# Kernel tuning notes

Measured on AMD Instinct MI355X. Metric: run time of the kernel, lower is better.

## Reference

```python
import jax, jax.numpy as jnp
import numpy as np

HAAR_K = 6  # kernel_size

def _haar_kernels_2d(k):
    # 6 classic Haar-like 2D kernels, each normalized by k*k (matches fixed
    # HaarFeatures2d conv weights): full box, 2-rect edges (h/v), 3-rect
    # lines (h/v), 4-rect checker.
    n = float(k * k)
    ks = []
    w = np.ones((k, k), np.float32); ks.append(w.copy())                      # full box
    w = np.ones((k, k), np.float32); w[k // 2:, :] = -1.0; ks.append(w)       # 2-rect vertical split
    w = np.ones((k, k), np.float32); w[:, k // 2:] = -1.0; ks.append(w)       # 2-rect horizontal split
    t = k // 3
    w = np.ones((k, k), np.float32); w[t:k - t, :] = -1.0; ks.append(w)       # 3-rect line (rows)
    w = np.ones((k, k), np.float32); w[:, t:k - t] = -1.0; ks.append(w)       # 3-rect line (cols)
    w = np.ones((k, k), np.float32)
    w[:k // 2, k // 2:] = -1.0; w[k // 2:, :k // 2] = -1.0; ks.append(w)      # 4-rect checker
    return jnp.asarray(np.stack(ks) / n)  # [6, k, k]


def setup_inputs() -> dict:
    key = jax.random.key(0)
    ks = jax.random.split(key, 4)
    def lin(k, o, i):  # kaiming-ish 1x1 conv weight as [out, in]
        return jax.random.normal(k, (o, i), jnp.float32) * (1.0 / np.sqrt(i))
    return {
        "x": jax.random.normal(ks[0], (16, 1, 512, 512), jnp.float32),
        "w1": lin(ks[1], 32, 6),  "b1": jnp.zeros((32,), jnp.float32),
        "w2": lin(ks[2], 16, 32), "b2": jnp.zeros((16,), jnp.float32),
        "w3": lin(ks[3], 2, 16),  "b3": jnp.zeros((2,), jnp.float32),
    }


def reference(x, w1, b1, w2, b2, w3, b3):
    # Fixed Haar-like feature extraction: conv with 6 constant kernels,
    # stride 1, 'same' zero padding. x: [B,1,H,W] -> f: [B,6,H,W]
    hk = _haar_kernels_2d(HAAR_K)[:, None]  # [6,1,k,k] OIHW
    f = jax.lax.conv_general_dilated(
        x, hk, window_strides=(1, 1), padding='SAME',
        dimension_numbers=('NCHW', 'OIHW', 'NCHW'))
    # 1x1-conv MLP classifier (Dropout2d is identity at inference)
    h = jax.nn.relu(jnp.einsum('bchw,oc->bohw', f, w1) + b1[None, :, None, None])
    h = jax.nn.relu(jnp.einsum('bchw,oc->bohw', h, w2) + b2[None, :, None, None])
    return jnp.einsum('bchw,oc->bohw', h, w3) + b3[None, :, None, None]  # [B,2,H,W]
```

## Files before the change

### kernel.cpp

```cpp
#include <hip/hip_runtime.h>


#define TW 64
#define TH 16

__global__ __launch_bounds__(512) void haar_prep(const float* __restrict__ w1,
                                                 const float* __restrict__ b1,
                                                 const float* __restrict__ w2,
                                                 float* __restrict__ ws) {
  int t = threadIdx.x;
  if (t < 256) {
    int m = t >> 3, k = t & 7;
    float v = 0.f;
    if (k < 6) v = w1[m * 6 + k] * (1.0f / 36.0f);
    else if (k == 6) v = b1[m];
    ws[t] = v;
  }
  int m = t >> 4, o = t & 15;
  ws[256 + t] = w2[o * 32 + m];
}

__global__ __launch_bounds__(256) void haar_main(const float* __restrict__ x,
                                                 const float* __restrict__ ws,
                                                 const float* __restrict__ b2,
                                                 const float* __restrict__ w3,
                                                 const float* __restrict__ b3,
                                                 float* __restrict__ out) {
  __shared__ float tile[TH + 5][72];

  const int tid = threadIdx.x;
  const int bc = blockIdx.x * TW;
  const int br = blockIdx.y * TH;
  const int b  = blockIdx.z;
  const float* xb = x + (size_t)b * (512 * 512);

  #pragma unroll
  for (int e = 0; e < 6; ++e) {
    int idx = tid + e * 256;
    if (idx < (TH + 5) * (TW + 5)) {
      int r = idx / (TW + 5);
      int c = idx - r * (TW + 5);
      int gr = br - 2 + r, gc = bc - 2 + c;
      float v = 0.f;
      if ((unsigned)gr < 512u && (unsigned)gc < 512u) v = xb[gr * 512 + gc];
      tile[r][c] = v;
    }
  }
  __syncthreads();

  const int jl = tid & 63;
  const int r0 = (tid >> 6) * 4;

  float A[9], S[9], T[9];
  #pragma unroll
  for (int rr = 0; rr < 9; ++rr) {
    const float* row = &tile[r0 + rr][jl];
    float x0 = row[0], x1 = row[1], x2 = row[2];
    float x3 = row[3], x4 = row[4], x5 = row[5];
    float p01 = x0 + x1, p23 = x2 + x3, p45 = x4 + x5;
    A[rr] = p01 + p23 + p45;
    T[rr] = p01 - p23 + p45;
    S[rr] = (p01 + x2) - (x3 + p45);
  }

  float f[6][4];
  #pragma unroll
  for (int p = 0; p < 4; ++p) {
    float ta = A[p] + A[p + 1] + A[p + 2];
    float tb = A[p + 3] + A[p + 4] + A[p + 5];
    f[0][p] = ta + tb;
    f[1][p] = ta - tb;
    float q01 = A[p] + A[p + 1], q23 = A[p + 2] + A[p + 3], q45 = A[p + 4] + A[p + 5];
    f[3][p] = q01 - q23 + q45;
    float sa = S[p] + S[p + 1] + S[p + 2];
    float sb = S[p + 3] + S[p + 4] + S[p + 5];
    f[2][p] = sa + sb;
    f[5][p] = sa - sb;
    f[4][p] = ((T[p] + T[p + 1]) + (T[p + 2] + T[p + 3])) + (T[p + 4] + T[p + 5]);
  }

  float h2[16][4];
  #pragma unroll
  for (int o = 0; o < 16; ++o) {
    float bv = b2[o];
    #pragma unroll
    for (int p = 0; p < 4; ++p) h2[o][p] = bv;
  }

  for (int m = 0; m < 32; ++m) {
    const float* pw1 = ws + m * 8;
    float w0 = pw1[0], w1v = pw1[1], w2v = pw1[2];
    float w3v = pw1[3], w4v = pw1[4], w5v = pw1[5], b1v = pw1[6];
    float t[4];
    #pragma unroll
    for (int p = 0; p < 4; ++p) {
      float a = fmaf(w0, f[0][p], b1v);
      a = fmaf(w1v, f[1][p], a);
      a = fmaf(w2v, f[2][p], a);
      a = fmaf(w3v, f[3][p], a);
      a = fmaf(w4v, f[4][p], a);
      a = fmaf(w5v, f[5][p], a);
      t[p] = fmaxf(a, 0.f);
    }
    const float* pw2 = ws + 256 + m * 16;
    #pragma unroll
    for (int o = 0; o < 16; ++o) {
      float wv = pw2[o];
      #pragma unroll
      for (int p = 0; p < 4; ++p) h2[o][p] = fmaf(wv, t[p], h2[o][p]);
    }
  }

  #pragma unroll
  for (int p = 0; p < 4; ++p) {
    float r[16];
    #pragma unroll
    for (int o = 0; o < 16; ++o) r[o] = fmaxf(h2[o][p], 0.f);
    #pragma unroll
    for (int u = 0; u < 2; ++u) {
      float acc = b3[u];
      #pragma unroll
      for (int o = 0; o < 16; ++o) acc = fmaf(w3[u * 16 + o], r[o], acc);
      size_t oidx = (((size_t)(b * 2 + u) * 512) + (br + r0 + p)) * 512 + (bc + jl);
      out[oidx] = acc;
    }
  }
}

extern "C" void kernel_launch(void* const* d_in, const int* in_sizes, int n_in,
                              void* d_out, int out_size, void* d_ws, size_t ws_size,
                              hipStream_t stream) {
  const float* x  = (const float*)d_in[0];
  const float* w1 = (const float*)d_in[1];
  const float* b1 = (const float*)d_in[2];
  const float* w2 = (const float*)d_in[3];
  const float* b2 = (const float*)d_in[4];
  const float* w3 = (const float*)d_in[5];
  const float* b3 = (const float*)d_in[6];
  float* out = (float*)d_out;
  float* ws  = (float*)d_ws;

  haar_prep<<<1, 512, 0, stream>>>(w1, b1, w2, ws);

  dim3 grid(512 / TW, 512 / TH, 16);
  haar_main<<<grid, 256, 0, stream>>>(x, ws, b2, w3, b3, out);
}
```

Measured before the change: 85.77 us.

## Process MLP per pixel sequentially and interleave weights into one workspace record

After: 87.41 us. About the same (+1.9%).

```diff
diff --git a/kernel.cpp b/kernel.cpp
--- a/kernel.cpp
+++ b/kernel.cpp
@@ -4,20 +4,17 @@
 #define TW 64
 #define TH 16
 
-__global__ __launch_bounds__(512) void haar_prep(const float* __restrict__ w1,
+__global__ __launch_bounds__(768) void haar_prep(const float* __restrict__ w1,
                                                  const float* __restrict__ b1,
                                                  const float* __restrict__ w2,
                                                  float* __restrict__ ws) {
   int t = threadIdx.x;
-  if (t < 256) {
-    int m = t >> 3, k = t & 7;
-    float v = 0.f;
-    if (k < 6) v = w1[m * 6 + k] * (1.0f / 36.0f);
-    else if (k == 6) v = b1[m];
-    ws[t] = v;
-  }
-  int m = t >> 4, o = t & 15;
-  ws[256 + t] = w2[o * 32 + m];
+  int m = t / 24, j = t % 24;
+  float v = 0.f;
+  if (j < 6)       v = w1[m * 6 + j] * (1.0f / 36.0f);
+  else if (j == 6) v = b1[m];
+  else if (j >= 8) v = w2[(j - 8) * 32 + m];
+  ws[m * 24 + j] = v;
 }
 
 __global__ __launch_bounds__(256) void haar_main(const float* __restrict__ x,
@@ -63,67 +60,56 @@
     S[rr] = (p01 + x2) - (x3 + p45);
   }
 
-  float f[6][4];
+  float f[4][6];
   #pragma unroll
   for (int p = 0; p < 4; ++p) {
     float ta = A[p] + A[p + 1] + A[p + 2];
     float tb = A[p + 3] + A[p + 4] + A[p + 5];
-    f[0][p] = ta + tb;
-    f[1][p] = ta - tb;
+    f[p][0] = ta + tb;
+    f[p][1] = ta - tb;
     float q01 = A[p] + A[p + 1], q23 = A[p + 2] + A[p + 3], q45 = A[p + 4] + A[p + 5];
-    f[3][p] = q01 - q23 + q45;
+    f[p][3] = q01 - q23 + q45;
     float sa = S[p] + S[p + 1] + S[p + 2];
     float sb = S[p + 3] + S[p + 4] + S[p + 5];
-    f[2][p] = sa + sb;
-    f[5][p] = sa - sb;
-    f[4][p] = ((T[p] + T[p + 1]) + (T[p + 2] + T[p + 3])) + (T[p + 4] + T[p + 5]);
+    f[p][2] = sa + sb;
+    f[p][5] = sa - sb;
+    f[p][4] = ((T[p] + T[p + 1]) + (T[p + 2] + T[p + 3])) + (T[p + 4] + T[p + 5]);
   }
 
-  float h2[16][4];
-  #pragma unroll
-  for (int o = 0; o < 16; ++o) {
-    float bv = b2[o];
-    #pragma unroll
-    for (int p = 0; p < 4; ++p) h2[o][p] = bv;
-  }
-
-  for (int m = 0; m < 32; ++m) {
-    const float* pw1 = ws + m * 8;
-    float w0 = pw1[0], w1v = pw1[1], w2v = pw1[2];
-    float w3v = pw1[3], w4v = pw1[4], w5v = pw1[5], b1v = pw1[6];
-    float t[4];
-    #pragma unroll
-    for (int p = 0; p < 4; ++p) {
-      float a = fmaf(w0, f[0][p], b1v);
-      a = fmaf(w1v, f[1][p], a);
-      a = fmaf(w2v, f[2][p], a);
-      a = fmaf(w3v, f[3][p], a);
-      a = fmaf(w4v, f[4][p], a);
-      a = fmaf(w5v, f[5][p], a);
-      t[p] = fmaxf(a, 0.f);
-    }
-    const float* pw2 = ws + 256 + m * 16;
-    #pragma unroll
-    for (int o = 0; o < 16; ++o) {
-      float wv = pw2[o];
-      #pragma unroll
-      for (int p = 0; p < 4; ++p) h2[o][p] = fmaf(wv, t[p], h2[o][p]);
-    }
-  }
+  const int colg = bc + jl;
 
   #pragma unroll
   for (int p = 0; p < 4; ++p) {
-    float r[16];
+    float h2[16];
     #pragma unroll
-    for (int o = 0; o < 16; ++o) r[o] = fmaxf(h2[o][p], 0.f);
+    for (int o = 0; o < 16; ++o) h2[o] = b2[o];
+
+    #pragma unroll 2
+    for (int m = 0; m < 32; ++m) {
+      const float* pm = ws + m * 24;
+      float a = pm[6];
+      a = fmaf(pm[0], f[p][0], a);
+      a = fmaf(pm[1], f[p][1], a);
+      a = fmaf(pm[2], f[p][2], a);
+      a = fmaf(pm[3], f[p][3], a);
+      a = fmaf(pm[4], f[p][4], a);
+      a = fmaf(pm[5], f[p][5], a);
+      a = fmaxf(a, 0.f);
+      #pragma unroll
+      for (int o = 0; o < 16; ++o) h2[o] = fmaf(pm[8 + o], a, h2[o]);
+    }
+
+    float acc0 = b3[0], acc1 = b3[1];
     #pragma unroll
-    for (int u = 0; u < 2; ++u) {
-      float acc = b3[u];
-      #pragma unroll
-      for (int o = 0; o < 16; ++o) acc = fmaf(w3[u * 16 + o], r[o], acc);
-      size_t oidx = (((size_t)(b * 2 + u) * 512) + (br + r0 + p)) * 512 + (bc + jl);
-      out[oidx] = acc;
+    for (int o = 0; o < 16; ++o) {
+      float r = fmaxf(h2[o], 0.f);
+      acc0 = fmaf(w3[o], r, acc0);
+      acc1 = fmaf(w3[16 + o], r, acc1);
     }
+
+    const int row = br + r0 + p;
+    out[((size_t)(b * 2 + 0) * 512 + row) * 512 + colg] = acc0;
+    out[((size_t)(b * 2 + 1) * 512 + row) * 512 + colg] = acc1;
   }
 }
 
@@ -140,7 +126,7 @@
   float* out = (float*)d_out;
   float* ws  = (float*)d_ws;
 
-  haar_prep<<<1, 512, 0, stream>>>(w1, b1, w2, ws);
+  haar_prep<<<1, 768, 0, stream>>>(w1, b1, w2, ws);
 
   dim3 grid(512 / TW, 512 / TH, 16);
   haar_main<<<grid, 256, 0, stream>>>(x, ws, b2, w3, b3, out);
```
